# Kernel tuning notes

Hardware: AMD Instinct MI355X
Metric: run time of the kernel (lower is better)

Reference implementation:

```python
import jax, jax.numpy as jnp
import numpy as np

B, T, N = 512, 1024, 48


def setup_inputs() -> dict:
    key = jax.random.key(0)
    k1, k2, k3, k4 = jax.random.split(key, 4)
    potentials = jax.random.normal(k1, (B, T, N), dtype=jnp.float32)
    y_true = jax.random.randint(k2, (B, T), 0, N, dtype=jnp.int32)
    lengths = jax.random.randint(k3, (B,), 1, T + 1, dtype=jnp.int32)
    transitions = jax.random.normal(k4, (N, N), dtype=jnp.float32)
    return {"potentials": potentials, "y_true": y_true,
            "lengths": lengths, "transitions": transitions}


def _crf_log_likelihood(potentials, tags, lengths, trans):
    # potentials: [B,T,N], tags: [B,T] int, lengths: [B] int, trans: [N,N]
    Bv, Tv, Nv = potentials.shape
    t_idx = jnp.arange(Tv)

    # ---- numerator: score of the given tag sequence ----
    unary = jnp.take_along_axis(potentials, tags[..., None], axis=2)[..., 0]  # [B,T]
    unary_mask = (t_idx[None, :] < lengths[:, None]).astype(potentials.dtype)
    unary_score = jnp.sum(unary * unary_mask, axis=1)  # [B]

    trans_scores = trans[tags[:, :-1], tags[:, 1:]]  # [B,T-1]
    pair_mask = (t_idx[None, 1:] < lengths[:, None]).astype(potentials.dtype)
    binary_score = jnp.sum(trans_scores * pair_mask, axis=1)  # [B]
    seq_score = unary_score + binary_score

    # ---- log partition: forward algorithm with length masking ----
    alpha0 = potentials[:, 0, :]  # [B,N]
    pots_rest = jnp.transpose(potentials[:, 1:, :], (1, 0, 2))  # [T-1,B,N]
    valid = (t_idx[1:, None] < lengths[None, :])  # [T-1,B]

    def step(alpha, inp):
        pot_t, v = inp  # [B,N], [B]
        # logsumexp over previous state: alpha[b,i] + trans[i,j]
        new_alpha = jax.nn.logsumexp(alpha[:, :, None] + trans[None, :, :], axis=1) + pot_t
        alpha = jnp.where(v[:, None], new_alpha, alpha)
        return alpha, None

    alpha_final, _ = jax.lax.scan(step, alpha0, (pots_rest, valid))
    log_norm = jax.nn.logsumexp(alpha_final, axis=-1)  # [B]

    return seq_score - log_norm


def reference(potentials, y_true, lengths, transitions):
    ll = _crf_log_likelihood(potentials, y_true.astype(jnp.int32),
                             lengths.astype(jnp.int32), transitions)
    return -ll  # per-sample NLL, shape [B]
```

## Files before the change

kernel.cpp:

```cpp
#include <hip/hip_runtime.h>
#include <cstdint>
#include <cstddef>

constexpr int Bb = 512;
constexpr int Tt = 1024;
constexpr int Nn = 48;
constexpr int SG = 16;
constexpr int NG = Bb / SG;
constexpr int Cc = 64;
constexpr int Lc = Tt / Cc;
constexpr int Wb = 32;
constexpr int TILE2 = 6400;
constexpr int NSLOT = 3;

typedef short bf16x8 __attribute__((ext_vector_type(8)));
typedef float f32x4  __attribute__((ext_vector_type(4)));
typedef unsigned int u32x4 __attribute__((ext_vector_type(4)));

__device__ __forceinline__ unsigned int bf16_rne(float x) {
    const unsigned int u = __float_as_uint(x);
    return ((u + 0x7FFFu + ((u >> 16) & 1u)) >> 16);
}
__device__ __forceinline__ unsigned int pack2(float lo, float hi) {
    return bf16_rne(lo) | (bf16_rne(hi) << 16);
}
__device__ __forceinline__ float safe_log(float x) {
    return __logf(fmaxf(x, 1e-30f));
}
__device__ __forceinline__ void gll16(const float* g, const char* l) {
    __builtin_amdgcn_global_load_lds(
        (const __attribute__((address_space(1))) void*)g,
        (__attribute__((address_space(3))) void*)l, 16, 0, 0);
}
#define DSR(dst, ad) asm volatile("ds_read_b128 %0, %1" : "=&v"(dst) : "v"(ad))

__launch_bounds__(64, 2)
__global__ void crf_fused(const float* __restrict__ pot,
                          const int*   __restrict__ ytrue,
                          const int*   __restrict__ lengths,
                          const float* __restrict__ trans,
                          float*       __restrict__ out)
{
    __shared__ __align__(16) char smem_c[NSLOT * TILE2];
    float* trans_lds = (float*)smem_c;

    const int lane = threadIdx.x;
    const int ln   = lane & 15;
    const int q    = lane >> 4;
    const int w    = blockIdx.x;
    const int gidx = (w & 7) * 4 + ((w >> 3) & 3);
    const int c    = w >> 5;
    const int s0   = gidx * SG;

    for (int i = lane; i < Nn * Nn; i += 64) trans_lds[i] = trans[i];
    __syncthreads();

    {
        const int    b    = w >> 2;
        const int    h    = w & 3;
        const int    lenb = lengths[b];
        const int*   yrow = ytrue + (size_t)b * Tt;
        const float* prow = pot + (size_t)b * Tt * Nn;
        float gold = 0.0f;
#pragma unroll
        for (int k = 0; k < Tt / 256; ++k) {
            const int   t    = h * (Tt / 4) + lane + 64 * k;
            const int   yt   = yrow[t];
            const int   ytm1 = yrow[(t > 0) ? (t - 1) : 0];
            const float u    = prow[(size_t)t * Nn + yt];
            const float tr   = trans_lds[ytm1 * Nn + yt];
            gold += (t < lenb) ? u : 0.0f;
            gold += (t >= 1 && t < lenb) ? tr : 0.0f;
        }
#pragma unroll
        for (int off = 32; off > 0; off >>= 1) gold += __shfl_xor(gold, off);
        if (lane == 0) atomicAdd(&out[b], -gold);
    }

    const int len_ln = lengths[s0 + ln];
    int lmax = len_ln;
#pragma unroll
    for (int off = 8; off > 0; off >>= 1) {
        const int o = __shfl_xor(lmax, off);
        lmax = (o > lmax) ? o : lmax;
    }

    const int start = (c == 0) ? 1 : c * Lc;
    if (c > 0 && start >= lmax) return;
    const int end = ((c + 1) * Lc < lmax) ? (c + 1) * Lc : lmax;

    bf16x8 Wf[3][2];
#pragma unroll
    for (int nt = 0; nt < 3; ++nt)
#pragma unroll
        for (int kc = 0; kc < 2; ++kc)
#pragma unroll
            for (int d = 0; d < 8; ++d) {
                int i;
                if (kc == 0) {
                    i = 16 * (d >> 2) + 4 * q + (d & 3);
                } else {
                    i = (d < 4) ? (32 + 4 * q + d) : -1;
                }
                const float v = (i >= 0) ? __expf(trans_lds[i * Nn + nt * 16 + ln]) : 0.0f;
                Wf[nt][kc][d] = (short)bf16_rne(v);
            }

    const int slC = ln;

    const float* prow = pot + (size_t)(s0 + ln) * (Tt * Nn);
    const float* pp0 = prow + 0 * 16 + q * 4;
    const float* pp1 = prow + 1 * 16 + q * 4;
    const float* pp2 = prow + 2 * 16 + q * 4;

    int t0 = (c == 0) ? 1 : (start - Wb);
    if (t0 < 1) t0 = 1;

    f32x4 pin0 = *(const f32x4*)(pp0 + (size_t)(t0 - 1) * Nn);
    f32x4 pin1 = *(const f32x4*)(pp1 + (size_t)(t0 - 1) * Nn);
    f32x4 pin2 = *(const f32x4*)(pp2 + (size_t)(t0 - 1) * Nn);
    const float cb0 = __shfl(pin0[0], slC);

    float gacc = (c == 0) ? cb0 : 0.0f;
    f32x4 prev0, prev1, prev2;
#pragma unroll
    for (int r = 0; r < 4; ++r) {
        prev0[r] = __expf(pin0[r] - cb0);
        prev1[r] = __expf(pin1[r] - cb0);
        prev2[r] = __expf(pin2[r] - cb0);
    }

    unsigned int pk00 = pack2(prev0[0], prev0[1]);
    unsigned int pk01 = pack2(prev0[2], prev0[3]);
    unsigned int pk10 = pack2(prev1[0], prev1[1]);
    unsigned int pk11 = pack2(prev1[2], prev1[3]);
    unsigned int pk20 = pack2(prev2[0], prev2[1]);
    unsigned int pk21 = pack2(prev2[2], prev2[3]);
    bf16x8 Bf0 = __builtin_bit_cast(bf16x8, (u32x4){pk00, pk01, pk10, pk11});
    bf16x8 Bf1 = __builtin_bit_cast(bf16x8, (u32x4){pk20, pk21, 0u, 0u});

    const float* srcp2[7];
#pragma unroll
    for (int i = 0; i < 7; ++i) {
        int sg = 64 * i + lane;
        int rr_ = sg / 25;  if (rr_ > 15) rr_ = 15;
        int cg  = sg % 25;  if (cg > 23) cg = 23;
        srcp2[i] = pot + (size_t)(s0 + rr_) * (Tt * Nn) + 4 * cg;
    }

    typedef __attribute__((address_space(3))) char as3char;
    const unsigned lbase  = (unsigned)(uintptr_t)(as3char*)smem_c;
    const unsigned adbase = lbase + (unsigned)(ln * 400 + q * 16);

    __syncthreads();

#define STAGE2(J, SLOT) do {                                                    \
        int tp_ = t0 + 2 * (J); if (tp_ > Tt - 2) tp_ = Tt - 2;                 \
        const size_t fo_ = (size_t)tp_ * Nn;                                    \
        char* lb_ = smem_c + (SLOT) * TILE2;                                    \
        gll16(srcp2[0] + fo_, lb_);                                             \
        gll16(srcp2[1] + fo_, lb_ + 1024);                                      \
        gll16(srcp2[2] + fo_, lb_ + 2048);                                      \
        gll16(srcp2[3] + fo_, lb_ + 3072);                                      \
        gll16(srcp2[4] + fo_, lb_ + 4096);                                      \
        gll16(srcp2[5] + fo_, lb_ + 5120);                                      \
        if (lane < 16) gll16(srcp2[6] + fo_, lb_ + 6144);                       \
    } while (0)

#define BOUNDARY(J, SLOT_NEXT) do {                                             \
        asm volatile("s_waitcnt vmcnt(7)");                                     \
        __builtin_amdgcn_sched_barrier(0);                                      \
        STAGE2((J) + 2, SLOT_NEXT);                                             \
    } while (0)

    float rrp = 1.0f;

    asm volatile("s_waitcnt vmcnt(0)");
    STAGE2(0, 0);
    STAGE2(1, 1);

    const int npr = ((((end - t0) + 1) >> 1) + 2) / 3 * 3;

#define CRF_STEP(KK, SLOT, SOFF)                                                \
    {                                                                           \
        const int t_ = t0 + (KK);                                               \
        f32x4 PA_, PB_, PC_;                                                    \
        const unsigned ad_ = adbase + (SLOT) * TILE2 + (SOFF);                  \
        DSR(PA_, ad_);                                                          \
        DSR(PB_, ad_ + 64u);                                                    \
        DSR(PC_, ad_ + 128u);                                                   \
        f32x4 z_ = {0.0f, 0.0f, 0.0f, 0.0f};                                    \
        f32x4 D0_ = __builtin_amdgcn_mfma_f32_16x16x32_bf16(Wf[0][0], Bf0, z_, 0, 0, 0); \
        f32x4 D1_ = __builtin_amdgcn_mfma_f32_16x16x32_bf16(Wf[1][0], Bf0, z_, 0, 0, 0); \
        f32x4 D2_ = __builtin_amdgcn_mfma_f32_16x16x32_bf16(Wf[2][0], Bf0, z_, 0, 0, 0); \
        D0_ = __builtin_amdgcn_mfma_f32_16x16x32_bf16(Wf[0][1], Bf1, D0_, 0, 0, 0); \
        D1_ = __builtin_amdgcn_mfma_f32_16x16x32_bf16(Wf[1][1], Bf1, D1_, 0, 0, 0); \
        D2_ = __builtin_amdgcn_mfma_f32_16x16x32_bf16(Wf[2][1], Bf1, D2_, 0, 0, 0); \
        asm volatile("s_waitcnt lgkmcnt(0)");                                   \
        __builtin_amdgcn_sched_barrier(0);                                      \
        f32x4 a0_, a1_, a2_;                                                    \
        _Pragma("unroll")                                                       \
        for (int r = 0; r < 4; ++r) {                                           \
            a0_[r] = D0_[r] * (__expf(PA_[r]) * rrp);                           \
            a1_[r] = D1_[r] * (__expf(PB_[r]) * rrp);                           \
            a2_[r] = D2_[r] * (__expf(PC_[r]) * rrp);                           \
        }                                                                       \
        const float cb_ = __shfl(a0_[0], slC);                                  \
        const float rr_ = __builtin_amdgcn_rcpf(fmaxf(cb_, 1e-30f));            \
        const float lg_ = safe_log(cb_);                                        \
        gacc += ((t_ >= start) && (t_ < end) && (t_ + 1 < len_ln)) ? lg_ : 0.0f; \
        const bool act_ = (t_ < len_ln);                                        \
        _Pragma("unroll")                                                       \
        for (int r = 0; r < 4; ++r) {                                           \
            prev0[r] = act_ ? a0_[r] : prev0[r];                                \
            prev1[r] = act_ ? a1_[r] : prev1[r];                                \
            prev2[r] = act_ ? a2_[r] : prev2[r];                                \
        }                                                                       \
        pk00 = pack2(prev0[0], prev0[1]);                                       \
        pk01 = pack2(prev0[2], prev0[3]);                                       \
        pk10 = pack2(prev1[0], prev1[1]);                                       \
        pk11 = pack2(prev1[2], prev1[3]);                                       \
        pk20 = pack2(prev2[0], prev2[1]);                                       \
        pk21 = pack2(prev2[2], prev2[3]);                                       \
        Bf0 = __builtin_bit_cast(bf16x8, (u32x4){pk00, pk01, pk10, pk11});      \
        Bf1 = __builtin_bit_cast(bf16x8, (u32x4){pk20, pk21, 0u, 0u});          \
        rrp = rr_;                                                              \
    }

    for (int j = 0; j < npr; j += 3) {
        BOUNDARY(j, 2);
        CRF_STEP(2 * j + 0, 0, 0);   CRF_STEP(2 * j + 1, 0, 192);
        BOUNDARY(j + 1, 0);
        CRF_STEP(2 * j + 2, 1, 0);   CRF_STEP(2 * j + 3, 1, 192);
        BOUNDARY(j + 2, 1);
        CRF_STEP(2 * j + 4, 2, 0);   CRF_STEP(2 * j + 5, 2, 192);
    }
#undef CRF_STEP
#undef BOUNDARY
#undef STAGE2

    asm volatile("s_waitcnt vmcnt(0)");

    float rs = prev0[0] + prev0[1] + prev0[2] + prev0[3]
             + prev1[0] + prev1[1] + prev1[2] + prev1[3]
             + prev2[0] + prev2[1] + prev2[2] + prev2[3];
    rs += __shfl_xor(rs, 16);
    rs += __shfl_xor(rs, 32);

    const bool active_chunk = (c == 0) || (c * Lc < len_ln);
    const bool last = active_chunk && (len_ln <= (c + 1) * Lc);
    const float G = gacc + (last ? safe_log(rs) : 0.0f);
    if (lane < 16) atomicAdd(&out[s0 + ln], G);
}

extern "C" void kernel_launch(void* const* d_in, const int* in_sizes, int n_in,
                              void* d_out, int out_size, void* d_ws, size_t ws_size,
                              hipStream_t stream)
{
    const float* pot   = (const float*)d_in[0];
    const int*   ytrue = (const int*)  d_in[1];
    const int*   lens  = (const int*)  d_in[2];
    const float* trans = (const float*)d_in[3];
    float*       out   = (float*)d_out;

    hipMemsetAsync(out, 0, (size_t)out_size * sizeof(float), stream);
    crf_fused<<<dim3(NG * Cc), dim3(64), 0, stream>>>(pot, ytrue, lens, trans, out);
}
```

Baseline: 185.5 us.

## Process two independent sequence groups per wave to interleave dependency chains

Each wavefront now carries two 16-sequence groups (A and B) through the forward recurrence at the same time. Their MFMA and exp/normalize tails are interleaved so each group's serial latency chain is hidden behind the other's. Shared-memory slots double in size and each stage issues twice as many global-to-LDS loads, with the vmcnt wait raised to match. The grid is halved and the launch-bounds occupancy hint is dropped. This adds register and LDS pressure, and the loop runs to the longer of the two groups' lengths.

```diff
diff --git a/kernel.cpp b/kernel.cpp
--- a/kernel.cpp
+++ b/kernel.cpp
@@ -11,6 +11,7 @@
 constexpr int Lc = Tt / Cc;
 constexpr int Wb = 32;
 constexpr int TILE2 = 6400;
+constexpr int SLOT2 = 2 * TILE2;
 constexpr int NSLOT = 3;
 
 typedef short bf16x8 __attribute__((ext_vector_type(8)));
@@ -34,37 +35,122 @@
 }
 #define DSR(dst, ad) asm volatile("ds_read_b128 %0, %1" : "=&v"(dst) : "v"(ad))
 
-__launch_bounds__(64, 2)
+struct Half {
+    f32x4 prev0, prev1, prev2;
+    bf16x8 Bf0, Bf1;
+    float gacc, rrp;
+    int len, end;
+};
+
+__device__ __forceinline__ void half_pack(Half& H) {
+    const unsigned k00 = pack2(H.prev0[0], H.prev0[1]);
+    const unsigned k01 = pack2(H.prev0[2], H.prev0[3]);
+    const unsigned k10 = pack2(H.prev1[0], H.prev1[1]);
+    const unsigned k11 = pack2(H.prev1[2], H.prev1[3]);
+    const unsigned k20 = pack2(H.prev2[0], H.prev2[1]);
+    const unsigned k21 = pack2(H.prev2[2], H.prev2[3]);
+    H.Bf0 = __builtin_bit_cast(bf16x8, (u32x4){k00, k01, k10, k11});
+    H.Bf1 = __builtin_bit_cast(bf16x8, (u32x4){k20, k21, 0u, 0u});
+}
+
+__device__ __forceinline__ void half_mfma(const bf16x8 (&Wf)[3][2], const Half& H,
+                                          f32x4& D0, f32x4& D1, f32x4& D2) {
+    f32x4 z = {0.0f, 0.0f, 0.0f, 0.0f};
+    D0 = __builtin_amdgcn_mfma_f32_16x16x32_bf16(Wf[0][0], H.Bf0, z, 0, 0, 0);
+    D1 = __builtin_amdgcn_mfma_f32_16x16x32_bf16(Wf[1][0], H.Bf0, z, 0, 0, 0);
+    D2 = __builtin_amdgcn_mfma_f32_16x16x32_bf16(Wf[2][0], H.Bf0, z, 0, 0, 0);
+    D0 = __builtin_amdgcn_mfma_f32_16x16x32_bf16(Wf[0][1], H.Bf1, D0, 0, 0, 0);
+    D1 = __builtin_amdgcn_mfma_f32_16x16x32_bf16(Wf[1][1], H.Bf1, D1, 0, 0, 0);
+    D2 = __builtin_amdgcn_mfma_f32_16x16x32_bf16(Wf[2][1], H.Bf1, D2, 0, 0, 0);
+}
+
+__device__ __forceinline__ void half_tail(Half& H, f32x4 D0, f32x4 D1, f32x4 D2,
+                                          f32x4 PA, f32x4 PB, f32x4 PC,
+                                          int t, int start, int slC) {
+    f32x4 a0, a1, a2;
+#pragma unroll
+    for (int r = 0; r < 4; ++r) {
+        a0[r] = D0[r] * (__expf(PA[r]) * H.rrp);
+        a1[r] = D1[r] * (__expf(PB[r]) * H.rrp);
+        a2[r] = D2[r] * (__expf(PC[r]) * H.rrp);
+    }
+    const float cb = __shfl(a0[0], slC);
+    const float rr = __builtin_amdgcn_rcpf(fmaxf(cb, 1e-30f));
+    const float lg = safe_log(cb);
+    H.gacc += ((t >= start) && (t < H.end) && (t + 1 < H.len)) ? lg : 0.0f;
+    const bool act = (t < H.len);
+#pragma unroll
+    for (int r = 0; r < 4; ++r) {
+        H.prev0[r] = act ? a0[r] : H.prev0[r];
+        H.prev1[r] = act ? a1[r] : H.prev1[r];
+        H.prev2[r] = act ? a2[r] : H.prev2[r];
+    }
+    half_pack(H);
+    H.rrp = rr;
+}
+
+__device__ __forceinline__ void half_init(Half& H, const float* pot, int s0h,
+                                          int ln, int q, int t0, int c) {
+    const size_t ROWS = (size_t)Tt * Nn;
+    const float* pr = pot + (size_t)(s0h + ln) * ROWS + (size_t)(t0 - 1) * Nn + q * 4;
+    const f32x4 p0 = *(const f32x4*)(pr);
+    const f32x4 p1 = *(const f32x4*)(pr + 16);
+    const f32x4 p2 = *(const f32x4*)(pr + 32);
+    const float cb0 = __shfl(p0[0], ln);
+    H.gacc = (c == 0) ? cb0 : 0.0f;
+#pragma unroll
+    for (int r = 0; r < 4; ++r) {
+        H.prev0[r] = __expf(p0[r] - cb0);
+        H.prev1[r] = __expf(p1[r] - cb0);
+        H.prev2[r] = __expf(p2[r] - cb0);
+    }
+    half_pack(H);
+    H.rrp = 1.0f;
+}
+
+__device__ __forceinline__ float half_final(const Half& H, int c) {
+    float rs = H.prev0[0] + H.prev0[1] + H.prev0[2] + H.prev0[3]
+             + H.prev1[0] + H.prev1[1] + H.prev1[2] + H.prev1[3]
+             + H.prev2[0] + H.prev2[1] + H.prev2[2] + H.prev2[3];
+    rs += __shfl_xor(rs, 16);
+    rs += __shfl_xor(rs, 32);
+    const bool active = (c == 0) || (c * Lc < H.len);
+    const bool last = active && (H.len <= (c + 1) * Lc);
+    return H.gacc + (last ? safe_log(rs) : 0.0f);
+}
+
+__launch_bounds__(64)
 __global__ void crf_fused(const float* __restrict__ pot,
                           const int*   __restrict__ ytrue,
                           const int*   __restrict__ lengths,
                           const float* __restrict__ trans,
                           float*       __restrict__ out)
 {
-    __shared__ __align__(16) char smem_c[NSLOT * TILE2];
+    __shared__ __align__(16) char smem_c[NSLOT * SLOT2];
     float* trans_lds = (float*)smem_c;
 
     const int lane = threadIdx.x;
     const int ln   = lane & 15;
     const int q    = lane >> 4;
     const int w    = blockIdx.x;
-    const int gidx = (w & 7) * 4 + ((w >> 3) & 3);
-    const int c    = w >> 5;
-    const int s0   = gidx * SG;
+    const int gA   = (w & 15) * 2;
+    const int c    = w >> 4;
+    const int s0A  = gA * SG;
+    const int s0B  = s0A + SG;
 
     for (int i = lane; i < Nn * Nn; i += 64) trans_lds[i] = trans[i];
     __syncthreads();
 
     {
-        const int    b    = w >> 2;
-        const int    h    = w & 3;
+        const int    b    = w >> 1;
+        const int    h    = w & 1;
         const int    lenb = lengths[b];
         const int*   yrow = ytrue + (size_t)b * Tt;
         const float* prow = pot + (size_t)b * Tt * Nn;
         float gold = 0.0f;
 #pragma unroll
-        for (int k = 0; k < Tt / 256; ++k) {
-            const int   t    = h * (Tt / 4) + lane + 64 * k;
+        for (int k = 0; k < Tt / 128; ++k) {
+            const int   t    = h * (Tt / 2) + lane + 64 * k;
             const int   yt   = yrow[t];
             const int   ytm1 = yrow[(t > 0) ? (t - 1) : 0];
             const float u    = prow[(size_t)t * Nn + yt];
@@ -77,17 +163,22 @@
         if (lane == 0) atomicAdd(&out[b], -gold);
     }
 
-    const int len_ln = lengths[s0 + ln];
-    int lmax = len_ln;
+    Half HA, HB;
+    HA.len = lengths[s0A + ln];
+    HB.len = lengths[s0B + ln];
+    int lmaxA = HA.len, lmaxB = HB.len;
 #pragma unroll
     for (int off = 8; off > 0; off >>= 1) {
-        const int o = __shfl_xor(lmax, off);
-        lmax = (o > lmax) ? o : lmax;
-    }
+        const int oa = __shfl_xor(lmaxA, off);  lmaxA = (oa > lmaxA) ? oa : lmaxA;
+        const int ob = __shfl_xor(lmaxB, off);  lmaxB = (ob > lmaxB) ? ob : lmaxB;
+    }
+    const int lmaxM = (lmaxA > lmaxB) ? lmaxA : lmaxB;
 
     const int start = (c == 0) ? 1 : c * Lc;
-    if (c > 0 && start >= lmax) return;
-    const int end = ((c + 1) * Lc < lmax) ? (c + 1) * Lc : lmax;
+    if (c > 0 && start >= lmaxM) return;
+    HA.end = ((c + 1) * Lc < lmaxA) ? (c + 1) * Lc : lmaxA;
+    HB.end = ((c + 1) * Lc < lmaxB) ? (c + 1) * Lc : lmaxB;
+    const int max_end = (HA.end > HB.end) ? HA.end : HB.end;
 
     bf16x8 Wf[3][2];
 #pragma unroll
@@ -97,55 +188,28 @@
 #pragma unroll
             for (int d = 0; d < 8; ++d) {
                 int i;
-                if (kc == 0) {
-                    i = 16 * (d >> 2) + 4 * q + (d & 3);
-                } else {
-                    i = (d < 4) ? (32 + 4 * q + d) : -1;
-                }
+                if (kc == 0) i = 16 * (d >> 2) + 4 * q + (d & 3);
+                else         i = (d < 4) ? (32 + 4 * q + d) : -1;
                 const float v = (i >= 0) ? __expf(trans_lds[i * Nn + nt * 16 + ln]) : 0.0f;
                 Wf[nt][kc][d] = (short)bf16_rne(v);
             }
-
     const int slC = ln;
-
-    const float* prow = pot + (size_t)(s0 + ln) * (Tt * Nn);
-    const float* pp0 = prow + 0 * 16 + q * 4;
-    const float* pp1 = prow + 1 * 16 + q * 4;
-    const float* pp2 = prow + 2 * 16 + q * 4;
 
     int t0 = (c == 0) ? 1 : (start - Wb);
     if (t0 < 1) t0 = 1;
 
-    f32x4 pin0 = *(const f32x4*)(pp0 + (size_t)(t0 - 1) * Nn);
-    f32x4 pin1 = *(const f32x4*)(pp1 + (size_t)(t0 - 1) * Nn);
-    f32x4 pin2 = *(const f32x4*)(pp2 + (size_t)(t0 - 1) * Nn);
-    const float cb0 = __shfl(pin0[0], slC);
-
-    float gacc = (c == 0) ? cb0 : 0.0f;
-    f32x4 prev0, prev1, prev2;
-#pragma unroll
-    for (int r = 0; r < 4; ++r) {
-        prev0[r] = __expf(pin0[r] - cb0);
-        prev1[r] = __expf(pin1[r] - cb0);
-        prev2[r] = __expf(pin2[r] - cb0);
-    }
-
-    unsigned int pk00 = pack2(prev0[0], prev0[1]);
-    unsigned int pk01 = pack2(prev0[2], prev0[3]);
-    unsigned int pk10 = pack2(prev1[0], prev1[1]);
-    unsigned int pk11 = pack2(prev1[2], prev1[3]);
-    unsigned int pk20 = pack2(prev2[0], prev2[1]);
-    unsigned int pk21 = pack2(prev2[2], prev2[3]);
-    bf16x8 Bf0 = __builtin_bit_cast(bf16x8, (u32x4){pk00, pk01, pk10, pk11});
-    bf16x8 Bf1 = __builtin_bit_cast(bf16x8, (u32x4){pk20, pk21, 0u, 0u});
-
-    const float* srcp2[7];
+    half_init(HA, pot, s0A, ln, q, t0, c);
+    half_init(HB, pot, s0B, ln, q, t0, c);
+
+    const size_t ROWS = (size_t)Tt * Nn;
+    const size_t DEL  = (size_t)SG * ROWS;
+    const float* srcA[7];
 #pragma unroll
     for (int i = 0; i < 7; ++i) {
         int sg = 64 * i + lane;
         int rr_ = sg / 25;  if (rr_ > 15) rr_ = 15;
         int cg  = sg % 25;  if (cg > 23) cg = 23;
-        srcp2[i] = pot + (size_t)(s0 + rr_) * (Tt * Nn) + 4 * cg;
+        srcA[i] = pot + (size_t)(s0A + rr_) * ROWS + 4 * cg;
     }
 
     typedef __attribute__((address_space(3))) char as3char;
@@ -157,100 +221,68 @@
 #define STAGE2(J, SLOT) do {                                                    \
         int tp_ = t0 + 2 * (J); if (tp_ > Tt - 2) tp_ = Tt - 2;                 \
         const size_t fo_ = (size_t)tp_ * Nn;                                    \
-        char* lb_ = smem_c + (SLOT) * TILE2;                                    \
-        gll16(srcp2[0] + fo_, lb_);                                             \
-        gll16(srcp2[1] + fo_, lb_ + 1024);                                      \
-        gll16(srcp2[2] + fo_, lb_ + 2048);                                      \
-        gll16(srcp2[3] + fo_, lb_ + 3072);                                      \
-        gll16(srcp2[4] + fo_, lb_ + 4096);                                      \
-        gll16(srcp2[5] + fo_, lb_ + 5120);                                      \
-        if (lane < 16) gll16(srcp2[6] + fo_, lb_ + 6144);                       \
+        char* la_ = smem_c + (SLOT) * SLOT2;                                    \
+        char* lb_ = la_ + TILE2;                                                \
+        gll16(srcA[0] + fo_, la_);            gll16(srcA[0] + DEL + fo_, lb_);  \
+        gll16(srcA[1] + fo_, la_ + 1024);     gll16(srcA[1] + DEL + fo_, lb_ + 1024); \
+        gll16(srcA[2] + fo_, la_ + 2048);     gll16(srcA[2] + DEL + fo_, lb_ + 2048); \
+        gll16(srcA[3] + fo_, la_ + 3072);     gll16(srcA[3] + DEL + fo_, lb_ + 3072); \
+        gll16(srcA[4] + fo_, la_ + 4096);     gll16(srcA[4] + DEL + fo_, lb_ + 4096); \
+        gll16(srcA[5] + fo_, la_ + 5120);     gll16(srcA[5] + DEL + fo_, lb_ + 5120); \
+        if (lane < 16) { gll16(srcA[6] + fo_, la_ + 6144);                      \
+                         gll16(srcA[6] + DEL + fo_, lb_ + 6144); }              \
     } while (0)
 
-#define BOUNDARY(J, SLOT_NEXT) do {                                             \
-        asm volatile("s_waitcnt vmcnt(7)");                                     \
+#define BOUNDARY(J, SLOTN) do {                                                 \
+        asm volatile("s_waitcnt vmcnt(14)");                                    \
         __builtin_amdgcn_sched_barrier(0);                                      \
-        STAGE2((J) + 2, SLOT_NEXT);                                             \
+        STAGE2((J) + 2, SLOTN);                                                 \
     } while (0)
 
-    float rrp = 1.0f;
+#define STEP2(SLOT, SOFF, TT)                                                   \
+    {                                                                           \
+        const int t_ = (TT);                                                    \
+        f32x4 PAa, PBa, PCa, PAb, PBb, PCb;                                     \
+        const unsigned adA_ = adbase + (SLOT) * SLOT2 + (SOFF);                 \
+        const unsigned adB_ = adA_ + TILE2;                                     \
+        DSR(PAa, adA_); DSR(PBa, adA_ + 64u); DSR(PCa, adA_ + 128u);            \
+        DSR(PAb, adB_); DSR(PBb, adB_ + 64u); DSR(PCb, adB_ + 128u);            \
+        f32x4 DA0, DA1, DA2, DB0, DB1, DB2;                                     \
+        half_mfma(Wf, HA, DA0, DA1, DA2);                                       \
+        half_mfma(Wf, HB, DB0, DB1, DB2);                                       \
+        asm volatile("s_waitcnt lgkmcnt(0)");                                   \
+        __builtin_amdgcn_sched_barrier(0);                                      \
+        half_tail(HA, DA0, DA1, DA2, PAa, PBa, PCa, t_, start, slC);            \
+        half_tail(HB, DB0, DB1, DB2, PAb, PBb, PCb, t_, start, slC);            \
+    }
 
     asm volatile("s_waitcnt vmcnt(0)");
     STAGE2(0, 0);
     STAGE2(1, 1);
 
-    const int npr = ((((end - t0) + 1) >> 1) + 2) / 3 * 3;
-
-#define CRF_STEP(KK, SLOT, SOFF)                                                \
-    {                                                                           \
-        const int t_ = t0 + (KK);                                               \
-        f32x4 PA_, PB_, PC_;                                                    \
-        const unsigned ad_ = adbase + (SLOT) * TILE2 + (SOFF);                  \
-        DSR(PA_, ad_);                                                          \
-        DSR(PB_, ad_ + 64u);                                                    \
-        DSR(PC_, ad_ + 128u);                                                   \
-        f32x4 z_ = {0.0f, 0.0f, 0.0f, 0.0f};                                    \
-        f32x4 D0_ = __builtin_amdgcn_mfma_f32_16x16x32_bf16(Wf[0][0], Bf0, z_, 0, 0, 0); \
-        f32x4 D1_ = __builtin_amdgcn_mfma_f32_16x16x32_bf16(Wf[1][0], Bf0, z_, 0, 0, 0); \
-        f32x4 D2_ = __builtin_amdgcn_mfma_f32_16x16x32_bf16(Wf[2][0], Bf0, z_, 0, 0, 0); \
-        D0_ = __builtin_amdgcn_mfma_f32_16x16x32_bf16(Wf[0][1], Bf1, D0_, 0, 0, 0); \
-        D1_ = __builtin_amdgcn_mfma_f32_16x16x32_bf16(Wf[1][1], Bf1, D1_, 0, 0, 0); \
-        D2_ = __builtin_amdgcn_mfma_f32_16x16x32_bf16(Wf[2][1], Bf1, D2_, 0, 0, 0); \
-        asm volatile("s_waitcnt lgkmcnt(0)");                                   \
-        __builtin_amdgcn_sched_barrier(0);                                      \
-        f32x4 a0_, a1_, a2_;                                                    \
-        _Pragma("unroll")                                                       \
-        for (int r = 0; r < 4; ++r) {                                           \
-            a0_[r] = D0_[r] * (__expf(PA_[r]) * rrp);                           \
-            a1_[r] = D1_[r] * (__expf(PB_[r]) * rrp);                           \
-            a2_[r] = D2_[r] * (__expf(PC_[r]) * rrp);                           \
-        }                                                                       \
-        const float cb_ = __shfl(a0_[0], slC);                                  \
-        const float rr_ = __builtin_amdgcn_rcpf(fmaxf(cb_, 1e-30f));            \
-        const float lg_ = safe_log(cb_);                                        \
-        gacc += ((t_ >= start) && (t_ < end) && (t_ + 1 < len_ln)) ? lg_ : 0.0f; \
-        const bool act_ = (t_ < len_ln);                                        \
-        _Pragma("unroll")                                                       \
-        for (int r = 0; r < 4; ++r) {                                           \
-            prev0[r] = act_ ? a0_[r] : prev0[r];                                \
-            prev1[r] = act_ ? a1_[r] : prev1[r];                                \
-            prev2[r] = act_ ? a2_[r] : prev2[r];                                \
-        }                                                                       \
-        pk00 = pack2(prev0[0], prev0[1]);                                       \
-        pk01 = pack2(prev0[2], prev0[3]);                                       \
-        pk10 = pack2(prev1[0], prev1[1]);                                       \
-        pk11 = pack2(prev1[2], prev1[3]);                                       \
-        pk20 = pack2(prev2[0], prev2[1]);                                       \
-        pk21 = pack2(prev2[2], prev2[3]);                                       \
-        Bf0 = __builtin_bit_cast(bf16x8, (u32x4){pk00, pk01, pk10, pk11});      \
-        Bf1 = __builtin_bit_cast(bf16x8, (u32x4){pk20, pk21, 0u, 0u});          \
-        rrp = rr_;                                                              \
-    }
+    const int pairs = ((max_end - t0) + 1) >> 1;
+    const int npr   = (pairs + 2) / 3 * 3;
 
     for (int j = 0; j < npr; j += 3) {
         BOUNDARY(j, 2);
-        CRF_STEP(2 * j + 0, 0, 0);   CRF_STEP(2 * j + 1, 0, 192);
+        STEP2(0, 0, t0 + 2 * j);     STEP2(0, 192, t0 + 2 * j + 1);
         BOUNDARY(j + 1, 0);
-        CRF_STEP(2 * j + 2, 1, 0);   CRF_STEP(2 * j + 3, 1, 192);
+        STEP2(1, 0, t0 + 2 * j + 2); STEP2(1, 192, t0 + 2 * j + 3);
         BOUNDARY(j + 2, 1);
-        CRF_STEP(2 * j + 4, 2, 0);   CRF_STEP(2 * j + 5, 2, 192);
-    }
-#undef CRF_STEP
+        STEP2(2, 0, t0 + 2 * j + 4); STEP2(2, 192, t0 + 2 * j + 5);
+    }
+#undef STEP2
 #undef BOUNDARY
 #undef STAGE2
 
     asm volatile("s_waitcnt vmcnt(0)");
 
-    float rs = prev0[0] + prev0[1] + prev0[2] + prev0[3]
-             + prev1[0] + prev1[1] + prev1[2] + prev1[3]
-             + prev2[0] + prev2[1] + prev2[2] + prev2[3];
-    rs += __shfl_xor(rs, 16);
-    rs += __shfl_xor(rs, 32);
-
-    const bool active_chunk = (c == 0) || (c * Lc < len_ln);
-    const bool last = active_chunk && (len_ln <= (c + 1) * Lc);
-    const float G = gacc + (last ? safe_log(rs) : 0.0f);
-    if (lane < 16) atomicAdd(&out[s0 + ln], G);
+    const float GA = half_final(HA, c);
+    const float GB = half_final(HB, c);
+    if (lane < 16) {
+        atomicAdd(&out[s0A + ln], GA);
+        atomicAdd(&out[s0B + ln], GB);
+    }
 }
 
 extern "C" void kernel_launch(void* const* d_in, const int* in_sizes, int n_in,
@@ -264,5 +296,5 @@
     float*       out   = (float*)d_out;
 
     hipMemsetAsync(out, 0, (size_t)out_size * sizeof(float), stream);
-    crf_fused<<<dim3(NG * Cc), dim3(64), 0, stream>>>(pot, ytrue, lens, trans, out);
-}
+    crf_fused<<<dim3(NG * Cc / 2), dim3(64), 0, stream>>>(pot, ytrue, lens, trans, out);
+}
```

New measurement: 189.2 us. 1.02x slower.
